# Optimization experiments

Hardware: AMD Instinct MI355X
Metric: run time of the kernel (lower is better)

The kernel has to match this reference:

```python
import jax, jax.numpy as jnp
import numpy as np

ALPHA = 1.702
LIMIT = 7.0
BLOCK = 32  # mxfp4 block size (values per scale)

# fp4 e2m1 lookup table, indexed by 4-bit code (sign in high bit)
FP4_LUT = jnp.array([0.0, 0.5, 1.0, 1.5, 2.0, 3.0, 4.0, 6.0,
                     -0.0, -0.5, -1.0, -1.5, -2.0, -3.0, -4.0, -6.0],
                    dtype=jnp.float32)


def dequant_mxfp4(blocks, scales):
    # blocks: [E, R, C//2] int byte values (two fp4 nibbles per byte, low nibble first)
    # scales: [E, R, C//32] e8m0 exponents; value = 2^(scale - 127)
    E, R, _ = blocks.shape
    nb = scales.shape[-1]
    lo = blocks & 0xF
    hi = (blocks >> 4) & 0xF
    vals = jnp.stack([FP4_LUT[lo], FP4_LUT[hi]], axis=-1)  # [E,R,C//2,2]
    vals = vals.reshape(E, R, nb, BLOCK)
    scale = jnp.exp2((scales - 127).astype(jnp.float32))   # [E,R,nb]
    return (vals * scale[..., None]).reshape(E, R, nb * BLOCK)  # [E,R,C]


def setup_inputs() -> dict:
    key = jax.random.key(0)
    ks = jax.random.split(key, 12)
    T, E, H, I = 1024, 8, 1024, 1024
    inp = {
        'hidden_states': jax.random.normal(ks[0], (T, H), dtype=jnp.float32),
        'router_logits': jax.random.normal(ks[1], (T, E), dtype=jnp.float32),
        'gate_proj_blocks': jax.random.randint(ks[2], (E, I, H // 2), 0, 256, dtype=jnp.int32),
        'gate_proj_scales': jax.random.randint(ks[3], (E, I, H // BLOCK), 121, 130, dtype=jnp.int32),
        'gate_proj_bias': jax.random.normal(ks[4], (E, I), dtype=jnp.float32) * 0.02,
        'up_proj_blocks': jax.random.randint(ks[5], (E, I, H // 2), 0, 256, dtype=jnp.int32),
        'up_proj_scales': jax.random.randint(ks[6], (E, I, H // BLOCK), 121, 130, dtype=jnp.int32),
        'up_proj_bias': jax.random.normal(ks[7], (E, I), dtype=jnp.float32) * 0.02,
        'down_proj_blocks': jax.random.randint(ks[8], (E, H, I // 2), 0, 256, dtype=jnp.int32),
        'down_proj_scales': jax.random.randint(ks[9], (E, H, I // BLOCK), 121, 130, dtype=jnp.int32),
        'down_proj_bias': jax.random.normal(ks[10], (E, H), dtype=jnp.float32) * 0.02,
        'k': 2,
    }
    return inp


def reference(hidden_states, router_logits, gate_proj_blocks, gate_proj_scales,
              gate_proj_bias, up_proj_blocks, up_proj_scales, up_proj_bias,
              down_proj_blocks, down_proj_scales, down_proj_bias, k):
    T, H = hidden_states.shape
    E = router_logits.shape[-1]
    # --- top-k routing: softmax over the selected logits, scattered to [T,E] ---
    top_vals, top_idx = jax.lax.top_k(router_logits, k)        # [T,k]
    top_w = jax.nn.softmax(top_vals, axis=-1)                   # [T,k]
    route = jnp.zeros((T, E), dtype=hidden_states.dtype)
    route = route.at[jnp.arange(T)[:, None], top_idx].add(top_w)  # [T,E]
    # --- dequantize mxfp4 expert weights ---
    gate_w = dequant_mxfp4(gate_proj_blocks, gate_proj_scales)  # [E,I,H]
    up_w = dequant_mxfp4(up_proj_blocks, up_proj_scales)        # [E,I,H]
    down_w = dequant_mxfp4(down_proj_blocks, down_proj_scales)  # [E,H,I]
    # --- GLU expert FFN (GPT-OSS variant) ---
    gate = jnp.einsum('th,eih->tei', hidden_states, gate_w) + gate_proj_bias[None]
    up = jnp.einsum('th,eih->tei', hidden_states, up_w) + up_proj_bias[None]
    gate = jnp.minimum(gate, LIMIT)
    up = jnp.clip(up, -LIMIT, LIMIT)
    glu = gate * jax.nn.sigmoid(gate * ALPHA)
    act = (up + 1.0) * glu                                       # [T,E,I]
    # fold routing weight in before the down projection, then sum over experts
    act = act * route[:, :, None]
    out = jnp.einsum('tei,ehi->th', act, down_w) + route @ down_proj_bias  # [T,H]
    return out
```

## Files before the change

### kernel.cpp

```cpp
#include <hip/hip_runtime.h>
#include <cstdint>
#include <cstddef>

typedef __bf16 bf16x8 __attribute__((ext_vector_type(8)));
typedef __bf16 bf16x2 __attribute__((ext_vector_type(2)));
typedef float f32x4 __attribute__((ext_vector_type(4)));
typedef unsigned short u16x2 __attribute__((ext_vector_type(2)));

constexpr int HH = 1024;
constexpr int II = 1024;
constexpr int KMAX = 2;
constexpr int EMAX = 8;
constexpr int GU_TILES = 40;
constexpr int DN_TILES = 40;
constexpr float FALPHA = 1.702f;
constexpr float FLIMIT = 7.0f;

#if __has_builtin(__builtin_amdgcn_cvt_scalef32_pk_bf16_fp4)
#define USE_CVT 1
#else
#define USE_CVT 0
#endif

#define SCHED0() __builtin_amdgcn_sched_barrier(0)

__device__ __forceinline__ unsigned pk_add16(unsigned a, unsigned b) {
  u16x2 x, y;
  __builtin_memcpy(&x, &a, 4); __builtin_memcpy(&y, &b, 4);
  u16x2 r = x + y;
  unsigned o; __builtin_memcpy(&o, &r, 4); return o;
}
__device__ __forceinline__ int4 decode_chunk(int4 raw, unsigned addk) {
  unsigned p = (unsigned)raw.x | ((unsigned)raw.y << 8) |
               ((unsigned)raw.z << 16) | ((unsigned)raw.w << 24);
  unsigned q = p >> 4;
  unsigned me = p & 0x07070707u, mo = q & 0x07070707u;
  unsigned se = p & 0x08080808u, so = q & 0x08080808u;
  unsigned hiE = __builtin_amdgcn_perm(0x40404040u, 0x3F3F3F14u, me) | (se << 4);
  unsigned hiO = __builtin_amdgcn_perm(0x40404040u, 0x3F3F3F14u, mo) | (so << 4);
  unsigned loE = __builtin_amdgcn_perm(0xC0804000u, 0xC0800000u, me);
  unsigned loO = __builtin_amdgcn_perm(0xC0804000u, 0xC0800000u, mo);
  int4 out;
  out.x = (int)pk_add16(__builtin_amdgcn_perm(hiE, loE, 0x05010400u), addk);
  out.y = (int)pk_add16(__builtin_amdgcn_perm(hiE, loE, 0x07030602u), addk);
  out.z = (int)pk_add16(__builtin_amdgcn_perm(hiO, loO, 0x05010400u), addk);
  out.w = (int)pk_add16(__builtin_amdgcn_perm(hiO, loO, 0x07030602u), addk);
  return out;
}
__device__ __forceinline__ unsigned make_addk(int s) {
  int k = s - 127;
  unsigned t = ((unsigned)(k << 7)) & 0xFFFFu;
  return t | (t << 16);
}

__device__ __forceinline__ bf16x8 decode_frag(int4 raw, int s) {
#if USE_CVT
  unsigned t0 = __builtin_amdgcn_perm((unsigned)raw.y, (unsigned)raw.x, 0x00000400u);
  unsigned t1 = __builtin_amdgcn_perm((unsigned)raw.w, (unsigned)raw.z, 0x00000400u);
  unsigned p  = __builtin_amdgcn_perm(t1, t0, 0x05040100u);
  float scf = __uint_as_float((unsigned)s << 23);
  bf16x2 a = __builtin_amdgcn_cvt_scalef32_pk_bf16_fp4(p, scf, 0);
  bf16x2 b = __builtin_amdgcn_cvt_scalef32_pk_bf16_fp4(p, scf, 1);
  bf16x2 c = __builtin_amdgcn_cvt_scalef32_pk_bf16_fp4(p, scf, 2);
  bf16x2 d = __builtin_amdgcn_cvt_scalef32_pk_bf16_fp4(p, scf, 3);
  bf16x8 r;
  r[0]=a[0]; r[1]=a[1]; r[2]=b[0]; r[3]=b[1]; r[4]=c[0]; r[5]=c[1]; r[6]=d[0]; r[7]=d[1];
  return r;
#else
  int4 d4 = decode_chunk(raw, make_addk(s));
  bf16x8 r; __builtin_memcpy(&r, &d4, 16);
  return r;
#endif
}

__device__ __forceinline__ void gll16(const void* g, void* l) {
  __builtin_amdgcn_global_load_lds(
      (const __attribute__((address_space(1))) void*)g,
      (__attribute__((address_space(3))) void*)l, 16, 0, 0);
}

__device__ __forceinline__ int xcd_swz(int wg, int nwg) {
  int q = nwg >> 3, r = nwg & 7;
  int xcd = wg & 7, pos = wg >> 3;
  return (xcd < r ? xcd * (q + 1) : r * (q + 1) + (xcd - r) * q) + pos;
}

__global__ __launch_bounds__(1024) void prep_kernel(
    const float* __restrict__ logits, const int* __restrict__ dk, int T, int E,
    float* __restrict__ route, float* __restrict__ tw,
    int* __restrict__ lists, int* __restrict__ counts,
    int* __restrict__ tabGU, int* __restrict__ tabDN) {
  __shared__ unsigned char s_ti[1024];
  __shared__ int s_cnt[EMAX];
  int t = threadIdx.x;
  int kk = *dk; if (kk > KMAX) kk = KMAX; if (kk < 1) kk = 1;
  int EE = E > EMAX ? EMAX : E;
  if (t < T) {
    float v[EMAX]; bool used[EMAX];
    for (int e = 0; e < EE; ++e) { v[e] = logits[t * E + e]; used[e] = false; route[t * E + e] = 0.f; }
    float tv[KMAX]; int ti[KMAX];
    for (int j = 0; j < kk; ++j) {
      float best = -3.4e38f; int bi = 0;
      for (int e = 0; e < EE; ++e) if (!used[e] && v[e] > best) { best = v[e]; bi = e; }
      used[bi] = true; tv[j] = best; ti[j] = bi;
    }
    float mx = tv[0], ssum = 0.f, wj[KMAX];
    for (int j = 0; j < kk; ++j) { wj[j] = __expf(tv[j] - mx); ssum += wj[j]; }
    for (int j = 0; j < kk; ++j) {
      float wv = wj[j] / ssum;
      route[t * E + ti[j]] = wv;
      tw[t * kk + j] = wv;
    }
    s_ti[t] = (unsigned char)(ti[0] | ((kk > 1 ? ti[1] : 0xF) << 4));
  } else if (t < 1024) {
    s_ti[t] = 0xFF;
  }
  __syncthreads();
  int w = t >> 6, lane = t & 63;
  if (w < EE) {
    int e = w, cnt = 0;
    for (int base = 0; base < T; base += 64) {
      int tt = base + lane;
      int j = -1;
      if (tt < T) {
        int packed = s_ti[tt];
        if ((packed & 0xF) == e) j = 0;
        else if ((packed >> 4) == e) j = 1;
      }
      unsigned long long m = __ballot(j >= 0);
      if (j >= 0) {
        int pre = __popcll(m & ((1ull << lane) - 1ull));
        lists[e * T + cnt + pre] = (tt << 3) | j;
      }
      cnt += __popcll(m);
    }
    if (lane == 0) { counts[e] = cnt; s_cnt[e] = cnt; }
  }
  __syncthreads();
  if (t == 0) {
    int g = 0, d = 0;
    for (int e = 0; e < EE; ++e) {
      int c = s_cnt[e];
      for (int m = 0; m * 64 < c && g < GU_TILES; ++m) tabGU[g++] = (e << 16) | m;
      for (int m = 0; m * 64 < c && d < DN_TILES; ++m) tabDN[d++] = (e << 16) | m;
    }
    for (; g < GU_TILES; ++g) tabGU[g] = -1;
    for (; d < DN_TILES; ++d) tabDN[d] = -1;
  }
}

__global__ void convert_hs(const float* __restrict__ hs, __bf16* __restrict__ hsb, int n8) {
  int g = blockIdx.x * 256 + threadIdx.x;
  if (g >= n8) return;
  const float4* p = (const float4*)hs + (size_t)g * 2;
  float4 a = p[0], b = p[1];
  bf16x8 r;
#if USE_CVT
  r[0] = (__bf16)a.x; r[1] = (__bf16)a.y; r[2] = (__bf16)a.z; r[3] = (__bf16)a.w;
  r[4] = (__bf16)b.x; r[5] = (__bf16)b.y; r[6] = (__bf16)b.z; r[7] = (__bf16)b.w;
#else
  r[0] = (__bf16)a.x; r[1] = (__bf16)a.z; r[2] = (__bf16)b.x; r[3] = (__bf16)b.z;
  r[4] = (__bf16)a.y; r[5] = (__bf16)a.w; r[6] = (__bf16)b.y; r[7] = (__bf16)b.w;
#endif
  *(bf16x8*)(hsb + (size_t)g * 8) = r;
}

__global__ __launch_bounds__(128, 4) void gemm_gate_up(
    const __bf16* __restrict__ hsb,
    const int* __restrict__ gblk, const int* __restrict__ gscl, const float* __restrict__ gbias,
    const int* __restrict__ ublk, const int* __restrict__ uscl, const float* __restrict__ ubias,
    const int* __restrict__ lists, const int* __restrict__ counts,
    const float* __restrict__ tw, const int* __restrict__ dk,
    const int* __restrict__ tab,
    __bf16* __restrict__ act, int T)
{
  int lin = xcd_swz(blockIdx.x, GU_TILES * (II / 16));
  int ntile = lin / GU_TILES, xt = lin % GU_TILES;
  int te = tab[xt];
  if (te < 0) return;
  int e = te >> 16, mtile = te & 0xFFFF;
  int cnt = counts[e];
  int n_valid = cnt - mtile * 64;
  if (n_valid <= 0) return;
  if (n_valid > 64) n_valid = 64;
  int kk = *dk; if (kk > KMAX) kk = KMAX; if (kk < 1) kk = 1;
  int ibase = ntile * 16;

  __shared__ int s_tok[64];
  __shared__ __attribute__((aligned(16))) char Abuf[2][8192];
  __shared__ __attribute__((aligned(16))) char Braw[2][4096];
  __shared__ __attribute__((aligned(8))) unsigned short sS[32][36];

  int tid = threadIdx.x;
  if (tid < 64) {
    int idx = mtile * 64 + tid;
    s_tok[tid] = lists[e * T + (idx < cnt ? idx : mtile * 64)];
  }
  __syncthreads();

  int lane = tid & 63, w = tid >> 6;
  int r15 = lane & 15, kg = lane >> 4;
  int cA = (lane & 7) ^ ((lane >> 3) & 7);

  unsigned aOff[4];
  #pragma unroll
  for (int q = 0; q < 4; ++q) {
    int row = w * 32 + q * 8 + (lane >> 3);
    int tok = s_tok[row] >> 3;
    aOff[q] = (unsigned)tok * (HH * 2) + (unsigned)cA * 16;
  }
  const char* bSrc[2];
  #pragma unroll
  for (int q = 0; q < 2; ++q) {
    int row = w * 16 + q * 8 + (lane >> 3);
    int mat = (row >> 4) & 1;
    int i = ibase + (row & 15);
    const int* base = mat ? ublk : gblk;
    bSrc[q] = (const char*)(base + ((size_t)e * II + i) * (HH / 2)) + cA * 16;
  }

  #pragma unroll
  for (int q = 0; q < 4; ++q)
    gll16((const char*)hsb + aOff[q], Abuf[0] + (w * 32 + q * 8) * 128);
  #pragma unroll
  for (int q = 0; q < 2; ++q)
    gll16(bSrc[q], Braw[0] + (w * 16 + q * 8) * 128);
  #pragma unroll
  for (int q = 0; q < 4; ++q)
    gll16((const char*)hsb + aOff[q] + 128, Abuf[1] + (w * 32 + q * 8) * 128);
  #pragma unroll
  for (int q = 0; q < 2; ++q)
    gll16(bSrc[q] + 128, Braw[1] + (w * 16 + q * 8) * 128);

  for (int idx = tid; idx < 256; idx += 128) {
    int row = idx >> 3, c4 = idx & 7;
    int mat = (row >> 4) & 1;
    int i = ibase + (row & 15);
    const int* sbase = mat ? uscl : gscl;
    int4 v = *((const int4*)(sbase + ((size_t)e * II + i) * 32) + c4);
    unsigned short* dst = &sS[row][c4 * 4];
    dst[0] = (unsigned short)v.x; dst[1] = (unsigned short)v.y;
    dst[2] = (unsigned short)v.z; dst[3] = (unsigned short)v.w;
  }
  __syncthreads();

  f32x4 acc[2][2];
  #pragma unroll
  for (int a = 0; a < 2; ++a) { acc[a][0] = (f32x4)0.f; acc[a][1] = (f32x4)0.f; }

  constexpr int NK = HH / 64;
  #pragma unroll 1
  for (int t = 0; t < NK; ++t) {
    if (t > 0) {
      if (t < NK - 1) { asm volatile("s_waitcnt vmcnt(6)" ::: "memory"); }
      else            { asm volatile("s_waitcnt vmcnt(0)" ::: "memory"); }
      SCHED0();
      __builtin_amdgcn_s_barrier();
      SCHED0();
    }
    const char* Ac = Abuf[t & 1];
    const char* Bc = Braw[t & 1];
    unsigned sv[2];
    sv[0] = *(const unsigned*)((const char*)sS + (r15) * 72 + t * 4);
    sv[1] = *(const unsigned*)((const char*)sS + (16 + r15) * 72 + t * 4);
    #pragma unroll
    for (int kq = 0; kq < 2; ++kq) {
      int kc = kq * 4 + kg;
      bf16x8 bfr[2];
      #pragma unroll
      for (int fn = 0; fn < 2; ++fn) {
        int n = fn * 16 + r15;
        int4 raw = *(const int4*)(Bc + n * 128 + ((kc ^ (n & 7)) << 4));
        int s = kq ? (int)(sv[fn] >> 16) : (int)(sv[fn] & 0xFFFF);
        bfr[fn] = decode_frag(raw, s);
      }
      #pragma unroll
      for (int fm = 0; fm < 2; ++fm) {
        int m = w * 32 + fm * 16 + r15;
        bf16x8 af = *(const bf16x8*)(Ac + m * 128 + ((kc ^ (m & 7)) << 4));
        acc[fm][0] = __builtin_amdgcn_mfma_f32_16x16x32_bf16(af, bfr[0], acc[fm][0], 0, 0, 0);
        acc[fm][1] = __builtin_amdgcn_mfma_f32_16x16x32_bf16(af, bfr[1], acc[fm][1], 0, 0, 0);
      }
    }
    if (t + 2 < NK) {
      asm volatile("s_waitcnt lgkmcnt(0)" ::: "memory");
      SCHED0();
      __builtin_amdgcn_s_barrier();
      SCHED0();
      char* An = Abuf[t & 1];
      char* Bn = Braw[t & 1];
      #pragma unroll
      for (int q = 0; q < 4; ++q)
        gll16((const char*)hsb + aOff[q] + (t + 2) * 128, An + (w * 32 + q * 8) * 128);
      #pragma unroll
      for (int q = 0; q < 2; ++q)
        gll16(bSrc[q] + (t + 2) * 128, Bn + (w * 16 + q * 8) * 128);
    }
  }

  {
    int i_log = ibase + r15;
    float gb = gbias[e * II + i_log], ub = ubias[e * II + i_log];
#if USE_CVT
    int i_st = i_log;
#else
    int i_st = (i_log & ~7) | ((i_log & 1) << 2) | ((i_log & 7) >> 1);
#endif
    #pragma unroll
    for (int fm = 0; fm < 2; ++fm) {
      #pragma unroll
      for (int rg = 0; rg < 4; ++rg) {
        int mloc = w * 32 + fm * 16 + kg * 4 + rg;
        if (mloc < n_valid) {
          int entry = s_tok[mloc];
          int t2 = entry >> 3, j = entry & 7;
          float wv = tw[t2 * kk + j];
          float g = fminf(acc[fm][0][rg] + gb, FLIMIT);
          float u = fminf(fmaxf(acc[fm][1][rg] + ub, -FLIMIT), FLIMIT);
          float glu = g / (1.f + __expf(-FALPHA * g));
          act[((size_t)t2 * kk + j) * II + i_st] = (__bf16)((u + 1.f) * glu * wv);
        }
      }
    }
  }
}

__global__ __launch_bounds__(128, 4) void gemm_down(
    const __bf16* __restrict__ act,
    const int* __restrict__ dblk, const int* __restrict__ dscl,
    const int* __restrict__ lists, const int* __restrict__ counts,
    const int* __restrict__ dk, const int* __restrict__ tab,
    __bf16* __restrict__ partial, int T)
{
  int lin = xcd_swz(blockIdx.x, DN_TILES * (HH / 32));
  int ntile = lin / DN_TILES, xt = lin % DN_TILES;
  int te = tab[xt];
  if (te < 0) return;
  int e = te >> 16, mtile = te & 0xFFFF;
  int cnt = counts[e];
  int n_valid = cnt - mtile * 64;
  if (n_valid <= 0) return;
  if (n_valid > 64) n_valid = 64;
  int kk = *dk; if (kk > KMAX) kk = KMAX; if (kk < 1) kk = 1;
  int hbase = ntile * 32;

  __shared__ int s_tok[64];
  __shared__ __attribute__((aligned(16))) char Abuf[2][8192];
  __shared__ __attribute__((aligned(16))) char Braw[2][4096];
  __shared__ __attribute__((aligned(8))) unsigned short sS[32][36];

  int tid = threadIdx.x;
  if (tid < 64) {
    int idx = mtile * 64 + tid;
    s_tok[tid] = lists[e * T + (idx < cnt ? idx : mtile * 64)];
  }
  __syncthreads();

  int lane = tid & 63, w = tid >> 6;
  int r15 = lane & 15, kg = lane >> 4;
  int cA = (lane & 7) ^ ((lane >> 3) & 7);

  unsigned aOff[4];
  #pragma unroll
  for (int q = 0; q < 4; ++q) {
    int row = w * 32 + q * 8 + (lane >> 3);
    int entry = s_tok[row];
    unsigned slot = (unsigned)(entry >> 3) * kk + (entry & 7);
    aOff[q] = slot * (II * 2) + (unsigned)cA * 16;
  }
  const char* bSrc[2];
  #pragma unroll
  for (int q = 0; q < 2; ++q) {
    int row = w * 16 + q * 8 + (lane >> 3);
    bSrc[q] = (const char*)(dblk + ((size_t)e * HH + hbase + row) * (II / 2)) + cA * 16;
  }

  #pragma unroll
  for (int q = 0; q < 4; ++q)
    gll16((const char*)act + aOff[q], Abuf[0] + (w * 32 + q * 8) * 128);
  #pragma unroll
  for (int q = 0; q < 2; ++q)
    gll16(bSrc[q], Braw[0] + (w * 16 + q * 8) * 128);
  #pragma unroll
  for (int q = 0; q < 4; ++q)
    gll16((const char*)act + aOff[q] + 128, Abuf[1] + (w * 32 + q * 8) * 128);
  #pragma unroll
  for (int q = 0; q < 2; ++q)
    gll16(bSrc[q] + 128, Braw[1] + (w * 16 + q * 8) * 128);

  for (int idx = tid; idx < 256; idx += 128) {
    int row = idx >> 3, c4 = idx & 7;
    int4 v = *((const int4*)(dscl + ((size_t)e * HH + hbase + row) * 32) + c4);
    unsigned short* dst = &sS[row][c4 * 4];
    dst[0] = (unsigned short)v.x; dst[1] = (unsigned short)v.y;
    dst[2] = (unsigned short)v.z; dst[3] = (unsigned short)v.w;
  }
  __syncthreads();

  f32x4 acc[2][2];
  #pragma unroll
  for (int a = 0; a < 2; ++a) { acc[a][0] = (f32x4)0.f; acc[a][1] = (f32x4)0.f; }

  constexpr int NK = II / 64;
  #pragma unroll 1
  for (int t = 0; t < NK; ++t) {
    if (t > 0) {
      if (t < NK - 1) { asm volatile("s_waitcnt vmcnt(6)" ::: "memory"); }
      else            { asm volatile("s_waitcnt vmcnt(0)" ::: "memory"); }
      SCHED0();
      __builtin_amdgcn_s_barrier();
      SCHED0();
    }
    const char* Ac = Abuf[t & 1];
    const char* Bc = Braw[t & 1];
    unsigned sv[2];
    sv[0] = *(const unsigned*)((const char*)sS + (r15) * 72 + t * 4);
    sv[1] = *(const unsigned*)((const char*)sS + (16 + r15) * 72 + t * 4);
    #pragma unroll
    for (int kq = 0; kq < 2; ++kq) {
      int kc = kq * 4 + kg;
      bf16x8 bfr[2];
      #pragma unroll
      for (int fn = 0; fn < 2; ++fn) {
        int n = fn * 16 + r15;
        int4 raw = *(const int4*)(Bc + n * 128 + ((kc ^ (n & 7)) << 4));
        int s = kq ? (int)(sv[fn] >> 16) : (int)(sv[fn] & 0xFFFF);
        bfr[fn] = decode_frag(raw, s);
      }
      #pragma unroll
      for (int fm = 0; fm < 2; ++fm) {
        int m = w * 32 + fm * 16 + r15;
        bf16x8 af = *(const bf16x8*)(Ac + m * 128 + ((kc ^ (m & 7)) << 4));
        acc[fm][0] = __builtin_amdgcn_mfma_f32_16x16x32_bf16(af, bfr[0], acc[fm][0], 0, 0, 0);
        acc[fm][1] = __builtin_amdgcn_mfma_f32_16x16x32_bf16(af, bfr[1], acc[fm][1], 0, 0, 0);
      }
    }
    if (t + 2 < NK) {
      asm volatile("s_waitcnt lgkmcnt(0)" ::: "memory");
      SCHED0();
      __builtin_amdgcn_s_barrier();
      SCHED0();
      char* An = Abuf[t & 1];
      char* Bn = Braw[t & 1];
      #pragma unroll
      for (int q = 0; q < 4; ++q)
        gll16((const char*)act + aOff[q] + (t + 2) * 128, An + (w * 32 + q * 8) * 128);
      #pragma unroll
      for (int q = 0; q < 2; ++q)
        gll16(bSrc[q] + (t + 2) * 128, Bn + (w * 16 + q * 8) * 128);
    }
  }

  #pragma unroll
  for (int fm = 0; fm < 2; ++fm) {
    #pragma unroll
    for (int rg = 0; rg < 4; ++rg) {
      int mloc = w * 32 + fm * 16 + kg * 4 + rg;
      if (mloc < n_valid) {
        int entry = s_tok[mloc];
        int t2 = entry >> 3, j = entry & 7;
        size_t slot = (size_t)t2 * kk + j;
        #pragma unroll
        for (int fn = 0; fn < 2; ++fn) {
          int h = hbase + fn * 16 + r15;
          partial[slot * HH + h] = (__bf16)acc[fm][fn][rg];
        }
      }
    }
  }
}

__global__ void combine_kernel(const __bf16* __restrict__ partial, const float* __restrict__ route,
                               const float* __restrict__ dbias, const int* __restrict__ dk,
                               float* __restrict__ out, int E) {
  int t = blockIdx.y;
  int h = blockIdx.x * 256 + threadIdx.x;
  int kk = *dk; if (kk > KMAX) kk = KMAX; if (kk < 1) kk = 1;
  float s = 0.f;
  for (int j = 0; j < kk; ++j) s += (float)partial[((size_t)t * kk + j) * HH + h];
  for (int e = 0; e < E; ++e) s += route[t * E + e] * dbias[(size_t)e * HH + h];
  out[(size_t)t * HH + h] = s;
}

extern "C" void kernel_launch(void* const* d_in, const int* in_sizes, int n_in,
                              void* d_out, int out_size, void* d_ws, size_t ws_size,
                              hipStream_t stream) {
  const float* hs    = (const float*)d_in[0];
  const float* rl    = (const float*)d_in[1];
  const int*   gblk  = (const int*)d_in[2];
  const int*   gscl  = (const int*)d_in[3];
  const float* gbias = (const float*)d_in[4];
  const int*   ublk  = (const int*)d_in[5];
  const int*   uscl  = (const int*)d_in[6];
  const float* ubias = (const float*)d_in[7];
  const int*   dblk  = (const int*)d_in[8];
  const int*   dscl  = (const int*)d_in[9];
  const float* dbias = (const float*)d_in[10];
  const int*   dk    = (const int*)d_in[11];

  long s0 = in_sizes[0], s1 = in_sizes[1], s2 = in_sizes[2], s4 = in_sizes[4];
  int H = (int)(2 * s2 / s4);
  int T = (int)(s0 / H);
  int E = (int)(s1 / T);

  char* w = (char*)d_ws;
  auto alloc = [&](size_t bytes) { char* p = w; w += (bytes + 255) & ~size_t(255); return p; };
  float*  route   = (float*)alloc(sizeof(float) * (size_t)T * E);
  float*  twp     = (float*)alloc(sizeof(float) * (size_t)T * KMAX);
  int*    counts  = (int*)  alloc(sizeof(int)   * (size_t)E);
  int*    lists   = (int*)  alloc(sizeof(int)   * (size_t)E * T);
  int*    tabGU   = (int*)  alloc(sizeof(int)   * GU_TILES);
  int*    tabDN   = (int*)  alloc(sizeof(int)   * DN_TILES);
  __bf16* hsb     = (__bf16*)alloc(sizeof(__bf16) * (size_t)T * HH);
  __bf16* act     = (__bf16*)alloc(sizeof(__bf16) * (size_t)T * KMAX * II);
  __bf16* partial = (__bf16*)alloc(sizeof(__bf16) * (size_t)T * KMAX * HH);

  prep_kernel<<<dim3(1), 1024, 0, stream>>>(rl, dk, T, E, route, twp, lists, counts, tabGU, tabDN);
  convert_hs<<<dim3((T * HH / 8 + 255) / 256), 256, 0, stream>>>(hs, hsb, T * HH / 8);
  gemm_gate_up<<<dim3(GU_TILES * (II / 16)), 128, 0, stream>>>(
      hsb, gblk, gscl, gbias, ublk, uscl, ubias, lists, counts, twp, dk, tabGU, act, T);
  gemm_down<<<dim3(DN_TILES * (HH / 32)), 128, 0, stream>>>(
      act, dblk, dscl, lists, counts, dk, tabDN, partial, T);
  combine_kernel<<<dim3(HH / 256, T), 256, 0, stream>>>(partial, route, dbias, dk, (float*)d_out, E);
}
```

Baseline: 97.24 us.

## Replace global_load_lds double buffering with register-staged prefetch; fuse prep and convert

Both grouped GEMMs stop using direct global-to-LDS loads into double-buffered shared memory. They now prefetch two K-steps ahead into registers and write them into a single LDS buffer between barriers, which halves LDS use and may improve occupancy. The routing prep and hidden-state bf16 conversion kernels are merged into one launch, with the last block doing the routing, to save a launch. The cost is extra VGPR pressure from the staging registers and more barriers per K-step.

```diff
diff --git a/kernel.cpp b/kernel.cpp
--- a/kernel.cpp
+++ b/kernel.cpp
@@ -73,23 +73,35 @@
 #endif
 }
 
-__device__ __forceinline__ void gll16(const void* g, void* l) {
-  __builtin_amdgcn_global_load_lds(
-      (const __attribute__((address_space(1))) void*)g,
-      (__attribute__((address_space(3))) void*)l, 16, 0, 0);
-}
-
 __device__ __forceinline__ int xcd_swz(int wg, int nwg) {
   int q = nwg >> 3, r = nwg & 7;
   int xcd = wg & 7, pos = wg >> 3;
   return (xcd < r ? xcd * (q + 1) : r * (q + 1) + (xcd - r) * q) + pos;
 }
 
-__global__ __launch_bounds__(1024) void prep_kernel(
+__global__ __launch_bounds__(1024) void prep_convert(
     const float* __restrict__ logits, const int* __restrict__ dk, int T, int E,
     float* __restrict__ route, float* __restrict__ tw,
     int* __restrict__ lists, int* __restrict__ counts,
-    int* __restrict__ tabGU, int* __restrict__ tabDN) {
+    int* __restrict__ tabGU, int* __restrict__ tabDN,
+    const float* __restrict__ hs, __bf16* __restrict__ hsb, int n8) {
+  if ((int)blockIdx.x < (int)gridDim.x - 1) {
+    int g = blockIdx.x * 1024 + threadIdx.x;
+    if (g < n8) {
+      const float4* p = (const float4*)hs + (size_t)g * 2;
+      float4 a = p[0], b = p[1];
+      bf16x8 r;
+#if USE_CVT
+      r[0] = (__bf16)a.x; r[1] = (__bf16)a.y; r[2] = (__bf16)a.z; r[3] = (__bf16)a.w;
+      r[4] = (__bf16)b.x; r[5] = (__bf16)b.y; r[6] = (__bf16)b.z; r[7] = (__bf16)b.w;
+#else
+      r[0] = (__bf16)a.x; r[1] = (__bf16)a.z; r[2] = (__bf16)b.x; r[3] = (__bf16)b.z;
+      r[4] = (__bf16)a.y; r[5] = (__bf16)a.w; r[6] = (__bf16)b.y; r[7] = (__bf16)b.w;
+#endif
+      *(bf16x8*)(hsb + (size_t)g * 8) = r;
+    }
+    return;
+  }
   __shared__ unsigned char s_ti[1024];
   __shared__ int s_cnt[EMAX];
   int t = threadIdx.x;
@@ -147,22 +159,6 @@
     for (; g < GU_TILES; ++g) tabGU[g] = -1;
     for (; d < DN_TILES; ++d) tabDN[d] = -1;
   }
-}
-
-__global__ void convert_hs(const float* __restrict__ hs, __bf16* __restrict__ hsb, int n8) {
-  int g = blockIdx.x * 256 + threadIdx.x;
-  if (g >= n8) return;
-  const float4* p = (const float4*)hs + (size_t)g * 2;
-  float4 a = p[0], b = p[1];
-  bf16x8 r;
-#if USE_CVT
-  r[0] = (__bf16)a.x; r[1] = (__bf16)a.y; r[2] = (__bf16)a.z; r[3] = (__bf16)a.w;
-  r[4] = (__bf16)b.x; r[5] = (__bf16)b.y; r[6] = (__bf16)b.z; r[7] = (__bf16)b.w;
-#else
-  r[0] = (__bf16)a.x; r[1] = (__bf16)a.z; r[2] = (__bf16)b.x; r[3] = (__bf16)b.z;
-  r[4] = (__bf16)a.y; r[5] = (__bf16)a.w; r[6] = (__bf16)b.y; r[7] = (__bf16)b.w;
-#endif
-  *(bf16x8*)(hsb + (size_t)g * 8) = r;
 }
 
 __global__ __launch_bounds__(128, 4) void gemm_gate_up(
@@ -187,8 +183,8 @@
   int ibase = ntile * 16;
 
   __shared__ int s_tok[64];
-  __shared__ __attribute__((aligned(16))) char Abuf[2][8192];
-  __shared__ __attribute__((aligned(16))) char Braw[2][4096];
+  __shared__ __attribute__((aligned(16))) char Abuf[8192];
+  __shared__ __attribute__((aligned(16))) char Braw[4096];
   __shared__ __attribute__((aligned(8))) unsigned short sS[32][36];
 
   int tid = threadIdx.x;
@@ -200,101 +196,136 @@
 
   int lane = tid & 63, w = tid >> 6;
   int r15 = lane & 15, kg = lane >> 4;
-  int cA = (lane & 7) ^ ((lane >> 3) & 7);
-
-  unsigned aOff[4];
+  int cL = lane & 7, sub = lane >> 3;
+  int cA = cL ^ sub;
+
+  const char* aSrc[4]; int aLds[4];
   #pragma unroll
   for (int q = 0; q < 4; ++q) {
-    int row = w * 32 + q * 8 + (lane >> 3);
+    int row = w * 32 + q * 8 + sub;
     int tok = s_tok[row] >> 3;
-    aOff[q] = (unsigned)tok * (HH * 2) + (unsigned)cA * 16;
-  }
-  const char* bSrc[2];
+    aSrc[q] = (const char*)hsb + (size_t)tok * (HH * 2) + cL * 16;
+    aLds[q] = row * 128 + (cA << 4);
+  }
+  const char* bSrc[2]; int bLds[2];
   #pragma unroll
   for (int q = 0; q < 2; ++q) {
-    int row = w * 16 + q * 8 + (lane >> 3);
+    int row = w * 16 + q * 8 + sub;
     int mat = (row >> 4) & 1;
     int i = ibase + (row & 15);
     const int* base = mat ? ublk : gblk;
-    bSrc[q] = (const char*)(base + ((size_t)e * II + i) * (HH / 2)) + cA * 16;
-  }
-
-  #pragma unroll
-  for (int q = 0; q < 4; ++q)
-    gll16((const char*)hsb + aOff[q], Abuf[0] + (w * 32 + q * 8) * 128);
-  #pragma unroll
-  for (int q = 0; q < 2; ++q)
-    gll16(bSrc[q], Braw[0] + (w * 16 + q * 8) * 128);
-  #pragma unroll
-  for (int q = 0; q < 4; ++q)
-    gll16((const char*)hsb + aOff[q] + 128, Abuf[1] + (w * 32 + q * 8) * 128);
-  #pragma unroll
-  for (int q = 0; q < 2; ++q)
-    gll16(bSrc[q] + 128, Braw[1] + (w * 16 + q * 8) * 128);
-
-  for (int idx = tid; idx < 256; idx += 128) {
-    int row = idx >> 3, c4 = idx & 7;
-    int mat = (row >> 4) & 1;
-    int i = ibase + (row & 15);
-    const int* sbase = mat ? uscl : gscl;
-    int4 v = *((const int4*)(sbase + ((size_t)e * II + i) * 32) + c4);
-    unsigned short* dst = &sS[row][c4 * 4];
-    dst[0] = (unsigned short)v.x; dst[1] = (unsigned short)v.y;
-    dst[2] = (unsigned short)v.z; dst[3] = (unsigned short)v.w;
-  }
-  __syncthreads();
+    bSrc[q] = (const char*)(base + ((size_t)e * II + i) * (HH / 2)) + cL * 16;
+    bLds[q] = row * 128 + (cA << 4);
+  }
+
+  {
+    int idx = tid;
+    #pragma unroll
+    for (int rep = 0; rep < 2; ++rep, idx += 128) {
+      int row = idx >> 3, c4 = idx & 7;
+      int mat = (row >> 4) & 1;
+      int i = ibase + (row & 15);
+      const int* sbase = mat ? uscl : gscl;
+      int4 v = *((const int4*)(sbase + ((size_t)e * II + i) * 32) + c4);
+      unsigned short* dst = &sS[row][c4 * 4];
+      dst[0] = (unsigned short)v.x; dst[1] = (unsigned short)v.y;
+      dst[2] = (unsigned short)v.z; dst[3] = (unsigned short)v.w;
+    }
+  }
 
   f32x4 acc[2][2];
   #pragma unroll
   for (int a = 0; a < 2; ++a) { acc[a][0] = (f32x4)0.f; acc[a][1] = (f32x4)0.f; }
 
+  int4 rA0[4], rA1[4], rB0[2], rB1[2];
+  #pragma unroll
+  for (int q = 0; q < 4; ++q) rA0[q] = *(const int4*)(aSrc[q]);
+  #pragma unroll
+  for (int q = 0; q < 2; ++q) rB0[q] = *(const int4*)(bSrc[q]);
+  #pragma unroll
+  for (int q = 0; q < 4; ++q) rA1[q] = *(const int4*)(aSrc[q] + 128);
+  #pragma unroll
+  for (int q = 0; q < 2; ++q) rB1[q] = *(const int4*)(bSrc[q] + 128);
+  asm volatile("s_waitcnt vmcnt(6)" ::: "memory");
+  SCHED0();
+  #pragma unroll
+  for (int q = 0; q < 4; ++q) *(int4*)(Abuf + aLds[q]) = rA0[q];
+  #pragma unroll
+  for (int q = 0; q < 2; ++q) *(int4*)(Braw + bLds[q]) = rB0[q];
+  asm volatile("s_waitcnt lgkmcnt(0)" ::: "memory");
+  SCHED0();
+  __builtin_amdgcn_s_barrier();
+
   constexpr int NK = HH / 64;
-  #pragma unroll 1
-  for (int t = 0; t < NK; ++t) {
-    if (t > 0) {
-      if (t < NK - 1) { asm volatile("s_waitcnt vmcnt(6)" ::: "memory"); }
-      else            { asm volatile("s_waitcnt vmcnt(0)" ::: "memory"); }
-      SCHED0();
-      __builtin_amdgcn_s_barrier();
-      SCHED0();
-    }
-    const char* Ac = Abuf[t & 1];
-    const char* Bc = Braw[t & 1];
-    unsigned sv[2];
-    sv[0] = *(const unsigned*)((const char*)sS + (r15) * 72 + t * 4);
-    sv[1] = *(const unsigned*)((const char*)sS + (16 + r15) * 72 + t * 4);
+
+  auto compute = [&](int t) {
+    unsigned sv0 = *(const unsigned*)((const char*)sS + (r15) * 72 + t * 4);
+    unsigned sv1 = *(const unsigned*)((const char*)sS + (16 + r15) * 72 + t * 4);
     #pragma unroll
     for (int kq = 0; kq < 2; ++kq) {
       int kc = kq * 4 + kg;
       bf16x8 bfr[2];
-      #pragma unroll
-      for (int fn = 0; fn < 2; ++fn) {
-        int n = fn * 16 + r15;
-        int4 raw = *(const int4*)(Bc + n * 128 + ((kc ^ (n & 7)) << 4));
-        int s = kq ? (int)(sv[fn] >> 16) : (int)(sv[fn] & 0xFFFF);
-        bfr[fn] = decode_frag(raw, s);
+      {
+        int n0 = r15;
+        int4 raw = *(const int4*)(Braw + n0 * 128 + ((kc ^ (n0 & 7)) << 4));
+        bfr[0] = decode_frag(raw, kq ? (int)(sv0 >> 16) : (int)(sv0 & 0xFFFF));
+        int n1 = 16 + r15;
+        int4 raw1 = *(const int4*)(Braw + n1 * 128 + ((kc ^ (n1 & 7)) << 4));
+        bfr[1] = decode_frag(raw1, kq ? (int)(sv1 >> 16) : (int)(sv1 & 0xFFFF));
       }
       #pragma unroll
       for (int fm = 0; fm < 2; ++fm) {
         int m = w * 32 + fm * 16 + r15;
-        bf16x8 af = *(const bf16x8*)(Ac + m * 128 + ((kc ^ (m & 7)) << 4));
+        bf16x8 af = *(const bf16x8*)(Abuf + m * 128 + ((kc ^ (m & 7)) << 4));
         acc[fm][0] = __builtin_amdgcn_mfma_f32_16x16x32_bf16(af, bfr[0], acc[fm][0], 0, 0, 0);
         acc[fm][1] = __builtin_amdgcn_mfma_f32_16x16x32_bf16(af, bfr[1], acc[fm][1], 0, 0, 0);
       }
     }
-    if (t + 2 < NK) {
+  };
+
+  #pragma unroll 1
+  for (int tt = 0; tt < NK; tt += 2) {
+    compute(tt);
+    __builtin_amdgcn_s_barrier();
+    SCHED0();
+    if (tt + 2 < NK) {
+      #pragma unroll
+      for (int q = 0; q < 4; ++q) rA0[q] = *(const int4*)(aSrc[q] + (tt + 2) * 128);
+      #pragma unroll
+      for (int q = 0; q < 2; ++q) rB0[q] = *(const int4*)(bSrc[q] + (tt + 2) * 128);
+      asm volatile("s_waitcnt vmcnt(6)" ::: "memory");
+    } else {
+      asm volatile("s_waitcnt vmcnt(0)" ::: "memory");
+    }
+    SCHED0();
+    #pragma unroll
+    for (int q = 0; q < 4; ++q) *(int4*)(Abuf + aLds[q]) = rA1[q];
+    #pragma unroll
+    for (int q = 0; q < 2; ++q) *(int4*)(Braw + bLds[q]) = rB1[q];
+    asm volatile("s_waitcnt lgkmcnt(0)" ::: "memory");
+    SCHED0();
+    __builtin_amdgcn_s_barrier();
+    compute(tt + 1);
+    if (tt + 2 < NK) {
+      __builtin_amdgcn_s_barrier();
+      SCHED0();
+      if (tt + 3 < NK) {
+        #pragma unroll
+        for (int q = 0; q < 4; ++q) rA1[q] = *(const int4*)(aSrc[q] + (tt + 3) * 128);
+        #pragma unroll
+        for (int q = 0; q < 2; ++q) rB1[q] = *(const int4*)(bSrc[q] + (tt + 3) * 128);
+        asm volatile("s_waitcnt vmcnt(6)" ::: "memory");
+      } else {
+        asm volatile("s_waitcnt vmcnt(0)" ::: "memory");
+      }
+      SCHED0();
+      #pragma unroll
+      for (int q = 0; q < 4; ++q) *(int4*)(Abuf + aLds[q]) = rA0[q];
+      #pragma unroll
+      for (int q = 0; q < 2; ++q) *(int4*)(Braw + bLds[q]) = rB0[q];
       asm volatile("s_waitcnt lgkmcnt(0)" ::: "memory");
       SCHED0();
       __builtin_amdgcn_s_barrier();
-      SCHED0();
-      char* An = Abuf[t & 1];
-      char* Bn = Braw[t & 1];
-      #pragma unroll
-      for (int q = 0; q < 4; ++q)
-        gll16((const char*)hsb + aOff[q] + (t + 2) * 128, An + (w * 32 + q * 8) * 128);
-      #pragma unroll
-      for (int q = 0; q < 2; ++q)
-        gll16(bSrc[q] + (t + 2) * 128, Bn + (w * 16 + q * 8) * 128);
     }
   }
 
@@ -345,8 +376,8 @@
   int hbase = ntile * 32;
 
   __shared__ int s_tok[64];
-  __shared__ __attribute__((aligned(16))) char Abuf[2][8192];
-  __shared__ __attribute__((aligned(16))) char Braw[2][4096];
+  __shared__ __attribute__((aligned(16))) char Abuf[8192];
+  __shared__ __attribute__((aligned(16))) char Braw[4096];
   __shared__ __attribute__((aligned(8))) unsigned short sS[32][36];
 
   int tid = threadIdx.x;
@@ -358,96 +389,131 @@
 
   int lane = tid & 63, w = tid >> 6;
   int r15 = lane & 15, kg = lane >> 4;
-  int cA = (lane & 7) ^ ((lane >> 3) & 7);
-
-  unsigned aOff[4];
+  int cL = lane & 7, sub = lane >> 3;
+  int cA = cL ^ sub;
+
+  const char* aSrc[4]; int aLds[4];
   #pragma unroll
   for (int q = 0; q < 4; ++q) {
-    int row = w * 32 + q * 8 + (lane >> 3);
+    int row = w * 32 + q * 8 + sub;
     int entry = s_tok[row];
-    unsigned slot = (unsigned)(entry >> 3) * kk + (entry & 7);
-    aOff[q] = slot * (II * 2) + (unsigned)cA * 16;
-  }
-  const char* bSrc[2];
+    size_t slot = (size_t)(entry >> 3) * kk + (entry & 7);
+    aSrc[q] = (const char*)act + slot * (II * 2) + cL * 16;
+    aLds[q] = row * 128 + (cA << 4);
+  }
+  const char* bSrc[2]; int bLds[2];
   #pragma unroll
   for (int q = 0; q < 2; ++q) {
-    int row = w * 16 + q * 8 + (lane >> 3);
-    bSrc[q] = (const char*)(dblk + ((size_t)e * HH + hbase + row) * (II / 2)) + cA * 16;
-  }
-
-  #pragma unroll
-  for (int q = 0; q < 4; ++q)
-    gll16((const char*)act + aOff[q], Abuf[0] + (w * 32 + q * 8) * 128);
-  #pragma unroll
-  for (int q = 0; q < 2; ++q)
-    gll16(bSrc[q], Braw[0] + (w * 16 + q * 8) * 128);
-  #pragma unroll
-  for (int q = 0; q < 4; ++q)
-    gll16((const char*)act + aOff[q] + 128, Abuf[1] + (w * 32 + q * 8) * 128);
-  #pragma unroll
-  for (int q = 0; q < 2; ++q)
-    gll16(bSrc[q] + 128, Braw[1] + (w * 16 + q * 8) * 128);
-
-  for (int idx = tid; idx < 256; idx += 128) {
-    int row = idx >> 3, c4 = idx & 7;
-    int4 v = *((const int4*)(dscl + ((size_t)e * HH + hbase + row) * 32) + c4);
-    unsigned short* dst = &sS[row][c4 * 4];
-    dst[0] = (unsigned short)v.x; dst[1] = (unsigned short)v.y;
-    dst[2] = (unsigned short)v.z; dst[3] = (unsigned short)v.w;
-  }
-  __syncthreads();
+    int row = w * 16 + q * 8 + sub;
+    bSrc[q] = (const char*)(dblk + ((size_t)e * HH + hbase + row) * (II / 2)) + cL * 16;
+    bLds[q] = row * 128 + (cA << 4);
+  }
+
+  {
+    int idx = tid;
+    #pragma unroll
+    for (int rep = 0; rep < 2; ++rep, idx += 128) {
+      int row = idx >> 3, c4 = idx & 7;
+      int4 v = *((const int4*)(dscl + ((size_t)e * HH + hbase + row) * 32) + c4);
+      unsigned short* dst = &sS[row][c4 * 4];
+      dst[0] = (unsigned short)v.x; dst[1] = (unsigned short)v.y;
+      dst[2] = (unsigned short)v.z; dst[3] = (unsigned short)v.w;
+    }
+  }
 
   f32x4 acc[2][2];
   #pragma unroll
   for (int a = 0; a < 2; ++a) { acc[a][0] = (f32x4)0.f; acc[a][1] = (f32x4)0.f; }
 
+  int4 rA0[4], rA1[4], rB0[2], rB1[2];
+  #pragma unroll
+  for (int q = 0; q < 4; ++q) rA0[q] = *(const int4*)(aSrc[q]);
+  #pragma unroll
+  for (int q = 0; q < 2; ++q) rB0[q] = *(const int4*)(bSrc[q]);
+  #pragma unroll
+  for (int q = 0; q < 4; ++q) rA1[q] = *(const int4*)(aSrc[q] + 128);
+  #pragma unroll
+  for (int q = 0; q < 2; ++q) rB1[q] = *(const int4*)(bSrc[q] + 128);
+  asm volatile("s_waitcnt vmcnt(6)" ::: "memory");
+  SCHED0();
+  #pragma unroll
+  for (int q = 0; q < 4; ++q) *(int4*)(Abuf + aLds[q]) = rA0[q];
+  #pragma unroll
+  for (int q = 0; q < 2; ++q) *(int4*)(Braw + bLds[q]) = rB0[q];
+  asm volatile("s_waitcnt lgkmcnt(0)" ::: "memory");
+  SCHED0();
+  __builtin_amdgcn_s_barrier();
+
   constexpr int NK = II / 64;
-  #pragma unroll 1
-  for (int t = 0; t < NK; ++t) {
-    if (t > 0) {
-      if (t < NK - 1) { asm volatile("s_waitcnt vmcnt(6)" ::: "memory"); }
-      else            { asm volatile("s_waitcnt vmcnt(0)" ::: "memory"); }
-      SCHED0();
-      __builtin_amdgcn_s_barrier();
-      SCHED0();
-    }
-    const char* Ac = Abuf[t & 1];
-    const char* Bc = Braw[t & 1];
-    unsigned sv[2];
-    sv[0] = *(const unsigned*)((const char*)sS + (r15) * 72 + t * 4);
-    sv[1] = *(const unsigned*)((const char*)sS + (16 + r15) * 72 + t * 4);
+
+  auto compute = [&](int t) {
+    unsigned sv0 = *(const unsigned*)((const char*)sS + (r15) * 72 + t * 4);
+    unsigned sv1 = *(const unsigned*)((const char*)sS + (16 + r15) * 72 + t * 4);
     #pragma unroll
     for (int kq = 0; kq < 2; ++kq) {
       int kc = kq * 4 + kg;
       bf16x8 bfr[2];
-      #pragma unroll
-      for (int fn = 0; fn < 2; ++fn) {
-        int n = fn * 16 + r15;
-        int4 raw = *(const int4*)(Bc + n * 128 + ((kc ^ (n & 7)) << 4));
-        int s = kq ? (int)(sv[fn] >> 16) : (int)(sv[fn] & 0xFFFF);
-        bfr[fn] = decode_frag(raw, s);
+      {
+        int n0 = r15;
+        int4 raw = *(const int4*)(Braw + n0 * 128 + ((kc ^ (n0 & 7)) << 4));
+        bfr[0] = decode_frag(raw, kq ? (int)(sv0 >> 16) : (int)(sv0 & 0xFFFF));
+        int n1 = 16 + r15;
+        int4 raw1 = *(const int4*)(Braw + n1 * 128 + ((kc ^ (n1 & 7)) << 4));
+        bfr[1] = decode_frag(raw1, kq ? (int)(sv1 >> 16) : (int)(sv1 & 0xFFFF));
       }
       #pragma unroll
       for (int fm = 0; fm < 2; ++fm) {
         int m = w * 32 + fm * 16 + r15;
-        bf16x8 af = *(const bf16x8*)(Ac + m * 128 + ((kc ^ (m & 7)) << 4));
+        bf16x8 af = *(const bf16x8*)(Abuf + m * 128 + ((kc ^ (m & 7)) << 4));
         acc[fm][0] = __builtin_amdgcn_mfma_f32_16x16x32_bf16(af, bfr[0], acc[fm][0], 0, 0, 0);
         acc[fm][1] = __builtin_amdgcn_mfma_f32_16x16x32_bf16(af, bfr[1], acc[fm][1], 0, 0, 0);
       }
     }
-    if (t + 2 < NK) {
+  };
+
+  #pragma unroll 1
+  for (int tt = 0; tt < NK; tt += 2) {
+    compute(tt);
+    __builtin_amdgcn_s_barrier();
+    SCHED0();
+    if (tt + 2 < NK) {
+      #pragma unroll
+      for (int q = 0; q < 4; ++q) rA0[q] = *(const int4*)(aSrc[q] + (tt + 2) * 128);
+      #pragma unroll
+      for (int q = 0; q < 2; ++q) rB0[q] = *(const int4*)(bSrc[q] + (tt + 2) * 128);
+      asm volatile("s_waitcnt vmcnt(6)" ::: "memory");
+    } else {
+      asm volatile("s_waitcnt vmcnt(0)" ::: "memory");
+    }
+    SCHED0();
+    #pragma unroll
+    for (int q = 0; q < 4; ++q) *(int4*)(Abuf + aLds[q]) = rA1[q];
+    #pragma unroll
+    for (int q = 0; q < 2; ++q) *(int4*)(Braw + bLds[q]) = rB1[q];
+    asm volatile("s_waitcnt lgkmcnt(0)" ::: "memory");
+    SCHED0();
+    __builtin_amdgcn_s_barrier();
+    compute(tt + 1);
+    if (tt + 2 < NK) {
+      __builtin_amdgcn_s_barrier();
+      SCHED0();
+      if (tt + 3 < NK) {
+        #pragma unroll
+        for (int q = 0; q < 4; ++q) rA1[q] = *(const int4*)(aSrc[q] + (tt + 3) * 128);
+        #pragma unroll
+        for (int q = 0; q < 2; ++q) rB1[q] = *(const int4*)(bSrc[q] + (tt + 3) * 128);
+        asm volatile("s_waitcnt vmcnt(6)" ::: "memory");
+      } else {
+        asm volatile("s_waitcnt vmcnt(0)" ::: "memory");
+      }
+      SCHED0();
+      #pragma unroll
+      for (int q = 0; q < 4; ++q) *(int4*)(Abuf + aLds[q]) = rA0[q];
+      #pragma unroll
+      for (int q = 0; q < 2; ++q) *(int4*)(Braw + bLds[q]) = rB0[q];
       asm volatile("s_waitcnt lgkmcnt(0)" ::: "memory");
       SCHED0();
       __builtin_amdgcn_s_barrier();
-      SCHED0();
-      char* An = Abuf[t & 1];
-      char* Bn = Braw[t & 1];
-      #pragma unroll
-      for (int q = 0; q < 4; ++q)
-        gll16((const char*)act + aOff[q] + (t + 2) * 128, An + (w * 32 + q * 8) * 128);
-      #pragma unroll
-      for (int q = 0; q < 2; ++q)
-        gll16(bSrc[q] + (t + 2) * 128, Bn + (w * 16 + q * 8) * 128);
     }
   }
 
@@ -515,8 +581,10 @@
   __bf16* act     = (__bf16*)alloc(sizeof(__bf16) * (size_t)T * KMAX * II);
   __bf16* partial = (__bf16*)alloc(sizeof(__bf16) * (size_t)T * KMAX * HH);
 
-  prep_kernel<<<dim3(1), 1024, 0, stream>>>(rl, dk, T, E, route, twp, lists, counts, tabGU, tabDN);
-  convert_hs<<<dim3((T * HH / 8 + 255) / 256), 256, 0, stream>>>(hs, hsb, T * HH / 8);
+  int n8 = T * HH / 8;
+  int nConv = (n8 + 1023) / 1024;
+  prep_convert<<<dim3(nConv + 1), 1024, 0, stream>>>(
+      rl, dk, T, E, route, twp, lists, counts, tabGU, tabDN, hs, hsb, n8);
   gemm_gate_up<<<dim3(GU_TILES * (II / 16)), 128, 0, stream>>>(
       hsb, gblk, gscl, gbias, ublk, uscl, ubias, lists, counts, twp, dk, tabGU, act, T);
   gemm_down<<<dim3(DN_TILES * (HH / 32)), 128, 0, stream>>>(
```

New measurement: 277.6 us. +185.5%, slower.
